# Kernel optimization log

Hardware: AMD Instinct MI355X
Metric: run time of the kernel (lower is better)

## Reference

```python
import jax, jax.numpy as jnp
import numpy as np

THETA = 10000.0

def precompute_freqs_cis(dim, seq_len):
    freqs = 1.0 / THETA ** (jnp.arange(0, dim, 2)[: dim // 2].astype(jnp.float32) / dim)
    t = jnp.arange(seq_len, dtype=jnp.float32)
    ang = jnp.outer(t, freqs)  # [T, dim/2]
    return jax.lax.complex(jnp.cos(ang), jnp.sin(ang))

def apply_rope(x, freqs_cis):
    # x: [..., T, D]; freqs_cis: [T, D/2] complex
    xr = x.astype(jnp.float32).reshape(*x.shape[:-1], -1, 2)
    xc = jax.lax.complex(xr[..., 0], xr[..., 1]) * freqs_cis
    out = jnp.stack([jnp.real(xc), jnp.imag(xc)], axis=-1).reshape(x.shape)
    return out.astype(x.dtype)

def setup_inputs() -> dict:
    key = jax.random.key(0)
    k1, k2, k3, k4 = jax.random.split(key, 4)
    B, T, E, DQ, DV = 4, 2048, 1024, 128, 128
    s = 1.0 / np.sqrt(E)
    return {
        "embedding_word": jax.random.normal(k1, (B, T, E), dtype=jnp.float32),
        "w_Q": jax.random.normal(k2, (DQ, E), dtype=jnp.float32) * s,  # torch Linear weight [out,in]
        "w_K": jax.random.normal(k3, (DQ, E), dtype=jnp.float32) * s,
        "w_V": jax.random.normal(k4, (DV, E), dtype=jnp.float32) * s,
    }

def reference(embedding_word, w_Q, w_K, w_V):
    T = embedding_word.shape[-2]
    dq = w_Q.shape[0]
    q = jnp.einsum("bte,de->btd", embedding_word, w_Q)
    k = jnp.einsum("bte,de->btd", embedding_word, w_K)
    v = jnp.einsum("bte,de->btd", embedding_word, w_V)
    fc = precompute_freqs_cis(dq, T)
    q = apply_rope(q, fc)
    k = apply_rope(k, fc)
    scores = jnp.einsum("bqd,bkd->bqk", q, k)
    causal = jnp.triu(jnp.ones((T, T), dtype=bool), k=1)
    masked = jnp.where(causal, -jnp.inf, scores)
    weights = jax.nn.softmax(masked / jnp.sqrt(jnp.float32(dq)), axis=-1)
    return jnp.einsum("bqk,bkd->bqd", weights, v)
```

## Files before the change

### kernel.cpp

```cpp
#include <hip/hip_runtime.h>
#include <math.h>


#define B_ 4
#define T_ 2048
#define E_ 1024
#define D_ 128
#define BT_ (B_ * T_)

#define UNITS_PER_B 160
#define UNITS (UNITS_PER_B * B_)

typedef __bf16 bf16_t;
typedef __bf16 bf16x4 __attribute__((ext_vector_type(4)));
typedef __bf16 bf16x8 __attribute__((ext_vector_type(8)));
typedef float f32x4 __attribute__((ext_vector_type(4)));

#define GLD16(g, l)                                                         \
  __builtin_amdgcn_global_load_lds(                                         \
      (const __attribute__((address_space(1))) void*)(g),                   \
      (__attribute__((address_space(3))) void*)(l), 16, 0, 0)

__device__ __forceinline__ bf16x8 cvt8(float4 lo, float4 hi) {
  bf16x8 t;
  t[0] = (bf16_t)lo.x; t[1] = (bf16_t)lo.y; t[2] = (bf16_t)lo.z; t[3] = (bf16_t)lo.w;
  t[4] = (bf16_t)hi.x; t[5] = (bf16_t)hi.y; t[6] = (bf16_t)hi.z; t[7] = (bf16_t)hi.w;
  return t;
}

__global__ __launch_bounds__(256) void precast_kernel(
    const float* __restrict__ X, const float* __restrict__ Wq,
    const float* __restrict__ Wk, const float* __restrict__ Wv,
    bf16_t* __restrict__ Xb, bf16_t* __restrict__ Wb,
    float2* __restrict__ Tab) {
  const int XC = BT_ * E_ / 8;
  const int WC = 3 * D_ * E_ / 8;
  for (int c = blockIdx.x * 256 + threadIdx.x; c < XC + WC;
       c += gridDim.x * 256) {
    const float* src;
    bf16_t* dst;
    if (c < XC) {
      src = X + (size_t)c * 8;
      dst = Xb + (size_t)c * 8;
    } else {
      const int cw = c - XC;
      const int z = cw / (D_ * E_ / 8);
      const int r = cw % (D_ * E_ / 8);
      src = ((z == 0) ? Wq : (z == 1) ? Wk : Wv) + (size_t)r * 8;
      dst = Wb + (size_t)z * D_ * E_ + (size_t)r * 8;
    }
    float4 u = *(const float4*)src;
    float4 v = *(const float4*)(src + 4);
    *(bf16x8*)dst = cvt8(u, v);
  }
  const float NLOG_ = -0.14391156514261485f;
  for (int idx = blockIdx.x * 256 + threadIdx.x; idx < T_ * 64;
       idx += gridDim.x * 256) {
    const int t = idx >> 6, j = idx & 63;
    const float freq = expf(NLOG_ * (float)j);
    float sn, cs;
    sincosf((float)t * freq, &sn, &cs);
    Tab[idx] = make_float2(cs, sn);
  }
}

__global__ __launch_bounds__(256) void proj64_kernel(
    const bf16_t* __restrict__ Xb, const bf16_t* __restrict__ Wb,
    const float2* __restrict__ Tab, bf16_t* __restrict__ Qws,
    bf16_t* __restrict__ Kws, bf16_t* __restrict__ Vtws) {
  const int o = blockIdx.x;
  const int ell = (o & 7) * 96 + (o >> 3);
  const int mt = ell / 6, ny = ell % 6;
  const int bt0 = mt * 64;

  const int tid = threadIdx.x;
  const int lane = tid & 63;
  const int wv = tid >> 6;
  const int wr = wv >> 1, wc = wv & 1;
  const int g = lane >> 4, lm = lane & 15;

  __shared__ bf16_t Ab[2][64 * 64];
  __shared__ bf16_t Bb[2][64 * 64];

  const bf16_t* Wz = Wb + (size_t)ny * 64 * E_;

  f32x4 acc[2][2];
#pragma unroll
  for (int m = 0; m < 2; m++)
#pragma unroll
    for (int n = 0; n < 2; n++) acc[m][n] = 0.0f;

  auto stage = [&](int t, int bf) {
    const int k0 = t * 64;
#pragma unroll
    for (int j = 0; j < 2; j++) {
      const int cb = (wv * 2 + j) * 64;
      const int c = cb + lane;
      const int row = c >> 3;
      const int eoff = ((c & 7) * 8) ^ ((row & 7) << 3);
      GLD16(Xb + (size_t)(bt0 + row) * E_ + k0 + eoff, &Ab[bf][cb * 8]);
    }
#pragma unroll
    for (int j = 0; j < 2; j++) {
      const int cb = (wv * 2 + j) * 64;
      const int c = cb + lane;
      const int row = c >> 3;
      const int eoff = ((c & 7) * 8) ^ ((row & 7) << 3);
      GLD16(Wz + (size_t)row * E_ + k0 + eoff, &Bb[bf][cb * 8]);
    }
  };

  auto compute = [&](int bf) {
#pragma unroll
    for (int ks = 0; ks < 2; ks++) {
      bf16x8 a0, a1, b0, b1;
      {
        const int r0 = wr * 32 + lm;
        a0 = *(const bf16x8*)&Ab[bf][r0 * 64 + ((ks * 32 + g * 8) ^ ((r0 & 7) << 3))];
        const int r1 = wr * 32 + 16 + lm;
        a1 = *(const bf16x8*)&Ab[bf][r1 * 64 + ((ks * 32 + g * 8) ^ ((r1 & 7) << 3))];
        const int s0 = wc * 32 + lm;
        b0 = *(const bf16x8*)&Bb[bf][s0 * 64 + ((ks * 32 + g * 8) ^ ((s0 & 7) << 3))];
        const int s1 = wc * 32 + 16 + lm;
        b1 = *(const bf16x8*)&Bb[bf][s1 * 64 + ((ks * 32 + g * 8) ^ ((s1 & 7) << 3))];
      }
      acc[0][0] = __builtin_amdgcn_mfma_f32_16x16x32_bf16(a0, b0, acc[0][0], 0, 0, 0);
      acc[0][1] = __builtin_amdgcn_mfma_f32_16x16x32_bf16(a0, b1, acc[0][1], 0, 0, 0);
      acc[1][0] = __builtin_amdgcn_mfma_f32_16x16x32_bf16(a1, b0, acc[1][0], 0, 0, 0);
      acc[1][1] = __builtin_amdgcn_mfma_f32_16x16x32_bf16(a1, b1, acc[1][1], 0, 0, 0);
    }
  };

  stage(0, 0);
  stage(1, 1);
  asm volatile("s_waitcnt vmcnt(4)" ::: "memory");
  __builtin_amdgcn_s_barrier();
  __builtin_amdgcn_sched_barrier(0);

#pragma unroll
  for (int t = 0; t < 16; t++) {
    compute(t & 1);
    __builtin_amdgcn_sched_barrier(0);
    __builtin_amdgcn_s_barrier();
    __builtin_amdgcn_sched_barrier(0);
    if (t + 2 < 16) {
      stage(t + 2, t & 1);
      asm volatile("s_waitcnt vmcnt(4)" ::: "memory");
    } else {
      asm volatile("s_waitcnt vmcnt(0)" ::: "memory");
    }
    __builtin_amdgcn_sched_barrier(0);
    __builtin_amdgcn_s_barrier();
    __builtin_amdgcn_sched_barrier(0);
  }

  const int b = bt0 >> 11;
#pragma unroll
  for (int nf = 0; nf < 2; nf++) {
    const int col = ny * 64 + wc * 32 + nf * 16 + lm;
    const int z = col >> 7;
    const int d = col & 127;
#pragma unroll
    for (int mf = 0; mf < 2; mf++) {
      const int row0 = bt0 + wr * 32 + mf * 16 + g * 4;
      if (z < 2) {
        bf16_t* dst = (z == 0) ? Qws : Kws;
#pragma unroll
        for (int r = 0; r < 4; r++) {
          const int bt = row0 + r;
          const int tt = bt & (T_ - 1);
          float val = acc[mf][nf][r];
          float prt = __shfl_xor(val, 1, 64);
          const float2 cs = Tab[(size_t)tt * 64 + (d >> 1)];
          const float outv =
              (d & 1) ? (prt * cs.y + val * cs.x) : (val * cs.x - prt * cs.y);
          dst[(size_t)bt * D_ + d] = (bf16_t)outv;
        }
      } else {
        bf16x4 pv;
#pragma unroll
        for (int r = 0; r < 4; r++) pv[r] = (bf16_t)acc[mf][nf][r];
        const int tt0 = row0 & (T_ - 1);
        *(bf16x4*)&Vtws[((size_t)(b * D_ + d)) * T_ + tt0] = pv;
      }
    }
  }
}

__global__ __launch_bounds__(128) void attn_part_kernel(
    const bf16_t* __restrict__ Qws, const bf16_t* __restrict__ Kws,
    const bf16_t* __restrict__ Vtws, float* __restrict__ Opart,
    float* __restrict__ Mpart, float* __restrict__ Lpart) {
  const int idx = blockIdx.x;
  const int b = idx / UNITS_PER_B;
  const int rem = idx % UNITS_PER_B;
  int qi, ci;
  if (rem < 16) { qi = rem; ci = 0; }
  else if (rem < 48) { int r2 = rem - 16; qi = 16 + (r2 >> 1); ci = r2 & 1; }
  else if (rem < 96) { int r2 = rem - 48; qi = 32 + r2 / 3; ci = r2 % 3; }
  else { int r2 = rem - 96; qi = 48 + (r2 >> 2); ci = r2 & 3; }
  const int slot = idx;

  const int q0 = qi * 32;
  const int tiles = (qi >> 1) + 1;
  const int t0 = ci * 8;
  const int t1 = min(t0 + 8, tiles);

  const int tid = threadIdx.x;
  const int lane = tid & 63;
  const int wv = tid >> 6;
  const int g = lane >> 4;
  const int lm = lane & 15;

  __shared__ bf16_t Ks[64 * 136];
  __shared__ bf16_t Vts[128 * 72];
  __shared__ bf16_t Ps[2 * 16 * 72];

  bf16x8 qf[4];
  {
    const bf16_t* qb = Qws + (size_t)(b * T_ + q0 + wv * 16 + lm) * D_;
#pragma unroll
    for (int kc = 0; kc < 4; kc++) qf[kc] = *(const bf16x8*)(qb + kc * 32 + g * 8);
  }

  f32x4 o[8];
#pragma unroll
  for (int i = 0; i < 8; i++) o[i] = 0.0f;
  float m_r[4], l_r[4];
#pragma unroll
  for (int r = 0; r < 4; r++) { m_r[r] = -1e30f; l_r[r] = 0.0f; }
  const float sc = 0.08838834764831845f;

  bf16x8 kreg[8], vreg[8];
  auto load_tiles = [&](int it) {
    const int k0 = it * 64;
#pragma unroll
    for (int i = 0; i < 8; i++) {
      const int c = tid + i * 128;
      kreg[i] = *(const bf16x8*)(Kws + (size_t)(b * T_ + k0 + (c >> 4)) * D_ +
                                 (c & 15) * 8);
    }
#pragma unroll
    for (int i = 0; i < 8; i++) {
      const int c = tid + i * 128;
      vreg[i] = *(const bf16x8*)(Vtws + (size_t)(b * D_ + (c >> 3)) * T_ + k0 +
                                 (c & 7) * 8);
    }
  };
  auto write_lds = [&]() {
#pragma unroll
    for (int i = 0; i < 8; i++) {
      const int c = tid + i * 128;
      *(bf16x8*)&Ks[(c >> 4) * 136 + (c & 15) * 8] = kreg[i];
    }
#pragma unroll
    for (int i = 0; i < 8; i++) {
      const int c = tid + i * 128;
      *(bf16x8*)&Vts[(c >> 3) * 72 + (c & 7) * 8] = vreg[i];
    }
  };

  load_tiles(t0);
  for (int it = t0; it < t1; it++) {
    write_lds();
    __syncthreads();
    if (it + 1 < t1) load_tiles(it + 1);

    const int k0 = it * 64;
    f32x4 s[4];
#pragma unroll
    for (int nb = 0; nb < 4; nb++) s[nb] = 0.0f;
#pragma unroll
    for (int nb = 0; nb < 4; nb++) {
#pragma unroll
      for (int kc = 0; kc < 4; kc++) {
        bf16x8 bk = *(const bf16x8*)&Ks[(nb * 16 + lm) * 136 + kc * 32 + g * 8];
        s[nb] = __builtin_amdgcn_mfma_f32_16x16x32_bf16(qf[kc], bk, s[nb], 0, 0, 0);
      }
    }

    const bool diag = (it == tiles - 1);
#pragma unroll
    for (int r = 0; r < 4; r++) {
      const int qrow = q0 + wv * 16 + g * 4 + r;
      float sv[4];
#pragma unroll
      for (int nb = 0; nb < 4; nb++) {
        sv[nb] = s[nb][r] * sc;
        if (diag && (k0 + nb * 16 + lm > qrow)) sv[nb] = -1e30f;
      }
      float tm = fmaxf(fmaxf(sv[0], sv[1]), fmaxf(sv[2], sv[3]));
      tm = fmaxf(tm, __shfl_xor(tm, 1, 64));
      tm = fmaxf(tm, __shfl_xor(tm, 2, 64));
      tm = fmaxf(tm, __shfl_xor(tm, 4, 64));
      tm = fmaxf(tm, __shfl_xor(tm, 8, 64));
      const float mnew = fmaxf(m_r[r], tm);
      const float alpha = __expf(m_r[r] - mnew);
      float p[4], rs = 0.0f;
#pragma unroll
      for (int nb = 0; nb < 4; nb++) { p[nb] = __expf(sv[nb] - mnew); rs += p[nb]; }
      rs += __shfl_xor(rs, 1, 64);
      rs += __shfl_xor(rs, 2, 64);
      rs += __shfl_xor(rs, 4, 64);
      rs += __shfl_xor(rs, 8, 64);
      l_r[r] = l_r[r] * alpha + rs;
      m_r[r] = mnew;
#pragma unroll
      for (int nb2 = 0; nb2 < 8; nb2++) o[nb2][r] *= alpha;
#pragma unroll
      for (int nb = 0; nb < 4; nb++)
        Ps[wv * 1152 + (g * 4 + r) * 72 + nb * 16 + lm] = (bf16_t)p[nb];
    }

    bf16x8 pa0 = *(const bf16x8*)&Ps[wv * 1152 + lm * 72 + g * 8];
    bf16x8 pa1 = *(const bf16x8*)&Ps[wv * 1152 + lm * 72 + 32 + g * 8];
#pragma unroll
    for (int nb2 = 0; nb2 < 8; nb2++) {
      bf16x8 bv0 = *(const bf16x8*)&Vts[(nb2 * 16 + lm) * 72 + g * 8];
      o[nb2] = __builtin_amdgcn_mfma_f32_16x16x32_bf16(pa0, bv0, o[nb2], 0, 0, 0);
      bf16x8 bv1 = *(const bf16x8*)&Vts[(nb2 * 16 + lm) * 72 + 32 + g * 8];
      o[nb2] = __builtin_amdgcn_mfma_f32_16x16x32_bf16(pa1, bv1, o[nb2], 0, 0, 0);
    }
    __syncthreads();
  }

#pragma unroll
  for (int r = 0; r < 4; r++) {
    const int row = wv * 16 + g * 4 + r;
    if (lm == 0) {
      Mpart[slot * 32 + row] = m_r[r];
      Lpart[slot * 32 + row] = l_r[r];
    }
    float* dst = Opart + ((size_t)slot * 32 + row) * D_;
#pragma unroll
    for (int nb2 = 0; nb2 < 8; nb2++) dst[nb2 * 16 + lm] = o[nb2][r];
  }
}

__global__ __launch_bounds__(256) void attn_combine_kernel(
    const float* __restrict__ Opart, const float* __restrict__ Mpart,
    const float* __restrict__ Lpart, float* __restrict__ Out) {
  const int qi = blockIdx.x;
  const int b = blockIdx.y;
  const int gg = qi >> 4;
  const int nc = gg + 1;
  const int base = b * UNITS_PER_B + ((gg * (gg + 1)) / 2) * 16 + (qi & 15) * nc;
  const int t = threadIdx.x;
  const int row = t >> 3;
  const int d0 = (t & 7) * 16;

  float mv[4];
  float mmax = -1e30f;
  for (int ci = 0; ci < nc; ci++) {
    mv[ci] = Mpart[(base + ci) * 32 + row];
    mmax = fmaxf(mmax, mv[ci]);
  }
  f32x4 acc[4];
#pragma unroll
  for (int j = 0; j < 4; j++) acc[j] = 0.0f;
  float l = 0.0f;
  for (int ci = 0; ci < nc; ci++) {
    const float w = __expf(mv[ci] - mmax);
    l += w * Lpart[(base + ci) * 32 + row];
    const float* op = Opart + ((size_t)(base + ci) * 32 + row) * D_ + d0;
#pragma unroll
    for (int j = 0; j < 4; j++) {
      float4 v = *(const float4*)(op + j * 4);
      acc[j][0] += w * v.x; acc[j][1] += w * v.y;
      acc[j][2] += w * v.z; acc[j][3] += w * v.w;
    }
  }
  const float inv = 1.0f / l;
  float* dst = Out + ((size_t)(b * T_ + qi * 32 + row)) * D_ + d0;
#pragma unroll
  for (int j = 0; j < 4; j++) {
    float4 v;
    v.x = acc[j][0] * inv; v.y = acc[j][1] * inv;
    v.z = acc[j][2] * inv; v.w = acc[j][3] * inv;
    *(float4*)(dst + j * 4) = v;
  }
}

__global__ __launch_bounds__(256) void proj_rope_kernel(
    const float* __restrict__ X, const float* __restrict__ Wq,
    const float* __restrict__ Wk, const float* __restrict__ Wv,
    bf16_t* __restrict__ Qws, bf16_t* __restrict__ Kws,
    bf16_t* __restrict__ Vtws) {
  const int z = blockIdx.y;
  const float* __restrict__ W = (z == 0) ? Wq : (z == 1) ? Wk : Wv;
  const int bt0 = blockIdx.x * 64;
  const int tid = threadIdx.x;
  const int lane = tid & 63;
  const int wv = tid >> 6;
  const int g = lane >> 4;
  const int lm = lane & 15;

  __shared__ bf16_t Xs[64 * 40];
  __shared__ bf16_t Ws[128 * 40];

  f32x4 acc[8];
#pragma unroll
  for (int i = 0; i < 8; i++) acc[i] = 0.0f;

  for (int kk = 0; kk < E_ / 32; kk++) {
    {
      const int row = tid >> 2, c0 = (tid & 3) * 8;
      const float* src = X + (size_t)(bt0 + row) * E_ + kk * 32 + c0;
      float4 u = *(const float4*)src;
      float4 v = *(const float4*)(src + 4);
      *(bf16x8*)&Xs[row * 40 + c0] = cvt8(u, v);
    }
#pragma unroll
    for (int h = 0; h < 2; h++) {
      const int cc = tid * 2 + h;
      const int row = cc >> 2, c0 = (cc & 3) * 8;
      const float* src = W + (size_t)row * E_ + kk * 32 + c0;
      float4 u = *(const float4*)src;
      float4 v = *(const float4*)(src + 4);
      *(bf16x8*)&Ws[row * 40 + c0] = cvt8(u, v);
    }
    __syncthreads();
    bf16x8 a = *(const bf16x8*)&Xs[(wv * 16 + lm) * 40 + g * 8];
#pragma unroll
    for (int nb = 0; nb < 8; nb++) {
      bf16x8 bb = *(const bf16x8*)&Ws[(nb * 16 + lm) * 40 + g * 8];
      acc[nb] = __builtin_amdgcn_mfma_f32_16x16x32_bf16(a, bb, acc[nb], 0, 0, 0);
    }
    __syncthreads();
  }
  const float NLOG_ = -0.14391156514261485f;
#pragma unroll
  for (int nb = 0; nb < 8; nb++) {
    const int col = nb * 16 + lm;
    const float freq = expf(NLOG_ * (float)(col >> 1));
#pragma unroll
    for (int r = 0; r < 4; r++) {
      const int bt = bt0 + wv * 16 + g * 4 + r;
      float val = acc[nb][r];
      float prt = __shfl_xor(val, 1, 64);
      if (z < 2) {
        const int t = bt & (T_ - 1);
        const float ang = (float)t * freq;
        float sn, cs;
        sincosf(ang, &sn, &cs);
        const float outv = (col & 1) ? (prt * sn + val * cs) : (val * cs - prt * sn);
        bf16_t* dst = (z == 0) ? Qws : Kws;
        dst[(size_t)bt * D_ + col] = (bf16_t)outv;
      } else {
        const int b = bt >> 11, t = bt & (T_ - 1);
        Vtws[((size_t)(b * D_ + col)) * T_ + t] = (bf16_t)val;
      }
    }
  }
}

__global__ __launch_bounds__(128) void attn_kernel(
    const bf16_t* __restrict__ Qws, const bf16_t* __restrict__ Kws,
    const bf16_t* __restrict__ Vtws, float* __restrict__ Out) {
  const int b = blockIdx.y;
  const int qi = blockIdx.x;
  const int q0 = qi * 32;
  const int tid = threadIdx.x;
  const int lane = tid & 63;
  const int wv = tid >> 6;
  const int g = lane >> 4;
  const int lm = lane & 15;

  __shared__ bf16_t Ks[32 * 136];
  __shared__ bf16_t Vts[128 * 40];
  __shared__ bf16_t Ps[2 * 16 * 40];

  bf16x8 qf[4];
  {
    const bf16_t* qb = Qws + (size_t)(b * T_ + q0 + wv * 16 + lm) * D_;
#pragma unroll
    for (int kk = 0; kk < 4; kk++) qf[kk] = *(const bf16x8*)(qb + kk * 32 + g * 8);
  }
  f32x4 o[8];
#pragma unroll
  for (int i = 0; i < 8; i++) o[i] = 0.0f;
  float m_r[4], l_r[4];
#pragma unroll
  for (int r = 0; r < 4; r++) { m_r[r] = -1e30f; l_r[r] = 0.0f; }
  const float sc = 0.08838834764831845f;

  for (int kt = 0; kt <= qi; kt++) {
    const int kv0 = kt * 32;
#pragma unroll
    for (int i = 0; i < 4; i++) {
      const int c = tid + i * 128;
      const int row = c >> 4, part = c & 15;
      bf16x8 v = *(const bf16x8*)(Kws + (size_t)(b * T_ + kv0 + row) * D_ + part * 8);
      *(bf16x8*)&Ks[row * 136 + part * 8] = v;
    }
#pragma unroll
    for (int i = 0; i < 4; i++) {
      const int c = tid + i * 128;
      const int d = c >> 2, part = c & 3;
      bf16x8 v = *(const bf16x8*)(Vtws + (size_t)(b * D_ + d) * T_ + kv0 + part * 8);
      *(bf16x8*)&Vts[d * 40 + part * 8] = v;
    }
    __syncthreads();
    f32x4 s[2];
    s[0] = 0.0f; s[1] = 0.0f;
#pragma unroll
    for (int nb = 0; nb < 2; nb++) {
#pragma unroll
      for (int kc = 0; kc < 4; kc++) {
        bf16x8 bk = *(const bf16x8*)&Ks[(nb * 16 + lm) * 136 + kc * 32 + g * 8];
        s[nb] = __builtin_amdgcn_mfma_f32_16x16x32_bf16(qf[kc], bk, s[nb], 0, 0, 0);
      }
    }
    const bool diag = (kt == qi);
#pragma unroll
    for (int r = 0; r < 4; r++) {
      float sv0 = s[0][r] * sc;
      float sv1 = s[1][r] * sc;
      if (diag) {
        const int rowr = wv * 16 + g * 4 + r;
        if (lm > rowr) sv0 = -1e30f;
        if (lm + 16 > rowr) sv1 = -1e30f;
      }
      float tm = fmaxf(sv0, sv1);
      tm = fmaxf(tm, __shfl_xor(tm, 1, 64));
      tm = fmaxf(tm, __shfl_xor(tm, 2, 64));
      tm = fmaxf(tm, __shfl_xor(tm, 4, 64));
      tm = fmaxf(tm, __shfl_xor(tm, 8, 64));
      const float mnew = fmaxf(m_r[r], tm);
      const float alpha = __expf(m_r[r] - mnew);
      const float p0 = __expf(sv0 - mnew);
      const float p1 = __expf(sv1 - mnew);
      float rs = p0 + p1;
      rs += __shfl_xor(rs, 1, 64);
      rs += __shfl_xor(rs, 2, 64);
      rs += __shfl_xor(rs, 4, 64);
      rs += __shfl_xor(rs, 8, 64);
      l_r[r] = l_r[r] * alpha + rs;
      m_r[r] = mnew;
#pragma unroll
      for (int nb2 = 0; nb2 < 8; nb2++) o[nb2][r] *= alpha;
      Ps[wv * 640 + (g * 4 + r) * 40 + lm] = (bf16_t)p0;
      Ps[wv * 640 + (g * 4 + r) * 40 + 16 + lm] = (bf16_t)p1;
    }
    bf16x8 pa = *(const bf16x8*)&Ps[wv * 640 + lm * 40 + g * 8];
#pragma unroll
    for (int nb2 = 0; nb2 < 8; nb2++) {
      bf16x8 bv = *(const bf16x8*)&Vts[(nb2 * 16 + lm) * 40 + g * 8];
      o[nb2] = __builtin_amdgcn_mfma_f32_16x16x32_bf16(pa, bv, o[nb2], 0, 0, 0);
    }
    __syncthreads();
  }
#pragma unroll
  for (int r = 0; r < 4; r++) {
    const float inv = 1.0f / l_r[r];
    float* dst = Out + (size_t)(b * T_ + q0 + wv * 16 + g * 4 + r) * D_;
#pragma unroll
    for (int nb2 = 0; nb2 < 8; nb2++) dst[nb2 * 16 + lm] = o[nb2][r] * inv;
  }
}

extern "C" void kernel_launch(void* const* d_in, const int* in_sizes, int n_in,
                              void* d_out, int out_size, void* d_ws,
                              size_t ws_size, hipStream_t stream) {
  const float* X = (const float*)d_in[0];
  const float* Wq = (const float*)d_in[1];
  const float* Wk = (const float*)d_in[2];
  const float* Wv = (const float*)d_in[3];
  float* Out = (float*)d_out;

  const size_t xb_bytes = (size_t)BT_ * E_ * sizeof(bf16_t);
  const size_t wb_bytes = (size_t)3 * D_ * E_ * sizeof(bf16_t);
  const size_t qkv_bytes = (size_t)3 * BT_ * D_ * sizeof(bf16_t);
  const size_t opart_bytes = (size_t)UNITS * 32 * D_ * sizeof(float);
  const size_t ml_bytes = (size_t)UNITS * 32 * sizeof(float);
  const size_t tab_bytes = (size_t)T_ * 64 * sizeof(float2);

  const size_t needA =
      xb_bytes + wb_bytes + qkv_bytes + opart_bytes + 2 * ml_bytes + tab_bytes;
  const size_t needB = qkv_bytes + opart_bytes + 2 * ml_bytes;

  if (ws_size >= needA) {
    bf16_t* Xb = (bf16_t*)d_ws;
    bf16_t* Wb = Xb + (size_t)BT_ * E_;
    bf16_t* Qws = Wb + (size_t)3 * D_ * E_;
    bf16_t* Kws = Qws + (size_t)BT_ * D_;
    bf16_t* Vtws = Kws + (size_t)BT_ * D_;
    float* Opart = (float*)((char*)d_ws + xb_bytes + wb_bytes + qkv_bytes);
    float* Mpart = (float*)((char*)Opart + opart_bytes);
    float* Lpart = (float*)((char*)Mpart + ml_bytes);
    float2* Tab = (float2*)((char*)Lpart + ml_bytes);

    hipLaunchKernelGGL(precast_kernel, dim3(2048), dim3(256), 0, stream,
                       X, Wq, Wk, Wv, Xb, Wb, Tab);
    hipLaunchKernelGGL(proj64_kernel, dim3(768), dim3(256), 0, stream,
                       Xb, Wb, Tab, Qws, Kws, Vtws);
    hipLaunchKernelGGL(attn_part_kernel, dim3(UNITS), dim3(128), 0, stream,
                       Qws, Kws, Vtws, Opart, Mpart, Lpart);
    hipLaunchKernelGGL(attn_combine_kernel, dim3(T_ / 32, B_), dim3(256), 0,
                       stream, Opart, Mpart, Lpart, Out);
  } else if (ws_size >= needB) {
    bf16_t* Qws = (bf16_t*)d_ws;
    bf16_t* Kws = Qws + (size_t)BT_ * D_;
    bf16_t* Vtws = Kws + (size_t)BT_ * D_;
    float* Opart = (float*)((char*)d_ws + qkv_bytes);
    float* Mpart = (float*)((char*)Opart + opart_bytes);
    float* Lpart = (float*)((char*)Mpart + ml_bytes);
    hipLaunchKernelGGL(proj_rope_kernel, dim3(BT_ / 64, 3), dim3(256), 0,
                       stream, X, Wq, Wk, Wv, Qws, Kws, Vtws);
    hipLaunchKernelGGL(attn_part_kernel, dim3(UNITS), dim3(128), 0, stream,
                       Qws, Kws, Vtws, Opart, Mpart, Lpart);
    hipLaunchKernelGGL(attn_combine_kernel, dim3(T_ / 32, B_), dim3(256), 0,
                       stream, Opart, Mpart, Lpart, Out);
  } else {
    bf16_t* Qws = (bf16_t*)d_ws;
    bf16_t* Kws = Qws + (size_t)BT_ * D_;
    bf16_t* Vtws = Kws + (size_t)BT_ * D_;
    hipLaunchKernelGGL(proj_rope_kernel, dim3(BT_ / 64, 3), dim3(256), 0,
                       stream, X, Wq, Wk, Wv, Qws, Kws, Vtws);
    hipLaunchKernelGGL(attn_kernel, dim3(T_ / 32, B_), dim3(128), 0, stream,
                       Qws, Kws, Vtws, Out);
  }
}
```

Measured before the change: 58.71 us.

## Fuse X fp32-to-bf16 conversion into projection GEMM staging

Removes the separate pass that converted the 32 MB fp32 activation tensor to bf16. The projection kernel now loads fp32 X tiles straight into LDS with a 16-chunk XOR swizzle and converts to bf16 when building MFMA fragments. The precast kernel is cut down to weights and the RoPE table only. In exchange, each projection block reads X in fp32 six times (once per output column tile), uses twice the LDS for the A tile, and adds conversion work to the inner loop.

```diff
diff --git a/kernel.cpp b/kernel.cpp
--- a/kernel.cpp
+++ b/kernel.cpp
@@ -27,35 +27,28 @@
   t[4] = (bf16_t)hi.x; t[5] = (bf16_t)hi.y; t[6] = (bf16_t)hi.z; t[7] = (bf16_t)hi.w;
   return t;
 }
-
-__global__ __launch_bounds__(256) void precast_kernel(
-    const float* __restrict__ X, const float* __restrict__ Wq,
-    const float* __restrict__ Wk, const float* __restrict__ Wv,
-    bf16_t* __restrict__ Xb, bf16_t* __restrict__ Wb,
+__device__ __forceinline__ bf16x8 cvt8v(f32x4 lo, f32x4 hi) {
+  bf16x8 t;
+  t[0] = (bf16_t)lo[0]; t[1] = (bf16_t)lo[1]; t[2] = (bf16_t)lo[2]; t[3] = (bf16_t)lo[3];
+  t[4] = (bf16_t)hi[0]; t[5] = (bf16_t)hi[1]; t[6] = (bf16_t)hi[2]; t[7] = (bf16_t)hi[3];
+  return t;
+}
+
+__global__ __launch_bounds__(256) void wtab_kernel(
+    const float* __restrict__ Wq, const float* __restrict__ Wk,
+    const float* __restrict__ Wv, bf16_t* __restrict__ Wb,
     float2* __restrict__ Tab) {
-  const int XC = BT_ * E_ / 8;
-  const int WC = 3 * D_ * E_ / 8;
-  for (int c = blockIdx.x * 256 + threadIdx.x; c < XC + WC;
-       c += gridDim.x * 256) {
-    const float* src;
-    bf16_t* dst;
-    if (c < XC) {
-      src = X + (size_t)c * 8;
-      dst = Xb + (size_t)c * 8;
-    } else {
-      const int cw = c - XC;
-      const int z = cw / (D_ * E_ / 8);
-      const int r = cw % (D_ * E_ / 8);
-      src = ((z == 0) ? Wq : (z == 1) ? Wk : Wv) + (size_t)r * 8;
-      dst = Wb + (size_t)z * D_ * E_ + (size_t)r * 8;
-    }
+  const int gidx = blockIdx.x * 256 + threadIdx.x;
+  if (gidx < 3 * D_ * E_ / 8) {
+    const int z = gidx / 16384;
+    const int r = gidx % 16384;
+    const float* src = ((z == 0) ? Wq : (z == 1) ? Wk : Wv) + (size_t)r * 8;
     float4 u = *(const float4*)src;
     float4 v = *(const float4*)(src + 4);
-    *(bf16x8*)dst = cvt8(u, v);
+    *(bf16x8*)(Wb + (size_t)z * D_ * E_ + (size_t)r * 8) = cvt8(u, v);
   }
   const float NLOG_ = -0.14391156514261485f;
-  for (int idx = blockIdx.x * 256 + threadIdx.x; idx < T_ * 64;
-       idx += gridDim.x * 256) {
+  for (int idx = gidx; idx < T_ * 64; idx += 65536) {
     const int t = idx >> 6, j = idx & 63;
     const float freq = expf(NLOG_ * (float)j);
     float sn, cs;
@@ -65,7 +58,7 @@
 }
 
 __global__ __launch_bounds__(256) void proj64_kernel(
-    const bf16_t* __restrict__ Xb, const bf16_t* __restrict__ Wb,
+    const float* __restrict__ X, const bf16_t* __restrict__ Wb,
     const float2* __restrict__ Tab, bf16_t* __restrict__ Qws,
     bf16_t* __restrict__ Kws, bf16_t* __restrict__ Vtws) {
   const int o = blockIdx.x;
@@ -79,7 +72,7 @@
   const int wr = wv >> 1, wc = wv & 1;
   const int g = lane >> 4, lm = lane & 15;
 
-  __shared__ bf16_t Ab[2][64 * 64];
+  __shared__ float Axf[2][64 * 64];
   __shared__ bf16_t Bb[2][64 * 64];
 
   const bf16_t* Wz = Wb + (size_t)ny * 64 * E_;
@@ -93,12 +86,13 @@
   auto stage = [&](int t, int bf) {
     const int k0 = t * 64;
 #pragma unroll
-    for (int j = 0; j < 2; j++) {
-      const int cb = (wv * 2 + j) * 64;
-      const int c = cb + lane;
-      const int row = c >> 3;
-      const int eoff = ((c & 7) * 8) ^ ((row & 7) << 3);
-      GLD16(Xb + (size_t)(bt0 + row) * E_ + k0 + eoff, &Ab[bf][cb * 8]);
+    for (int j = 0; j < 4; j++) {
+      const int cb = (wv * 4 + j) * 64;
+      const int L = cb + lane;
+      const int row = L >> 4;
+      const int pch = L & 15;
+      const int c = pch ^ (row & 15);
+      GLD16(X + (size_t)(bt0 + row) * E_ + k0 + c * 4, &Axf[bf][cb * 4]);
     }
 #pragma unroll
     for (int j = 0; j < 2; j++) {
@@ -113,12 +107,17 @@
   auto compute = [&](int bf) {
 #pragma unroll
     for (int ks = 0; ks < 2; ks++) {
+      const int cc = ks * 8 + g * 2;
       bf16x8 a0, a1, b0, b1;
       {
         const int r0 = wr * 32 + lm;
-        a0 = *(const bf16x8*)&Ab[bf][r0 * 64 + ((ks * 32 + g * 8) ^ ((r0 & 7) << 3))];
+        f32x4 lo0 = *(const f32x4*)&Axf[bf][r0 * 64 + (cc ^ (r0 & 15)) * 4];
+        f32x4 hi0 = *(const f32x4*)&Axf[bf][r0 * 64 + ((cc + 1) ^ (r0 & 15)) * 4];
+        a0 = cvt8v(lo0, hi0);
         const int r1 = wr * 32 + 16 + lm;
-        a1 = *(const bf16x8*)&Ab[bf][r1 * 64 + ((ks * 32 + g * 8) ^ ((r1 & 7) << 3))];
+        f32x4 lo1 = *(const f32x4*)&Axf[bf][r1 * 64 + (cc ^ (r1 & 15)) * 4];
+        f32x4 hi1 = *(const f32x4*)&Axf[bf][r1 * 64 + ((cc + 1) ^ (r1 & 15)) * 4];
+        a1 = cvt8v(lo1, hi1);
         const int s0 = wc * 32 + lm;
         b0 = *(const bf16x8*)&Bb[bf][s0 * 64 + ((ks * 32 + g * 8) ^ ((s0 & 7) << 3))];
         const int s1 = wc * 32 + 16 + lm;
@@ -133,7 +132,7 @@
 
   stage(0, 0);
   stage(1, 1);
-  asm volatile("s_waitcnt vmcnt(4)" ::: "memory");
+  asm volatile("s_waitcnt vmcnt(6)" ::: "memory");
   __builtin_amdgcn_s_barrier();
   __builtin_amdgcn_sched_barrier(0);
 
@@ -145,7 +144,7 @@
     __builtin_amdgcn_sched_barrier(0);
     if (t + 2 < 16) {
       stage(t + 2, t & 1);
-      asm volatile("s_waitcnt vmcnt(4)" ::: "memory");
+      asm volatile("s_waitcnt vmcnt(6)" ::: "memory");
     } else {
       asm volatile("s_waitcnt vmcnt(0)" ::: "memory");
     }
@@ -568,7 +567,6 @@
   const float* Wv = (const float*)d_in[3];
   float* Out = (float*)d_out;
 
-  const size_t xb_bytes = (size_t)BT_ * E_ * sizeof(bf16_t);
   const size_t wb_bytes = (size_t)3 * D_ * E_ * sizeof(bf16_t);
   const size_t qkv_bytes = (size_t)3 * BT_ * D_ * sizeof(bf16_t);
   const size_t opart_bytes = (size_t)UNITS * 32 * D_ * sizeof(float);
@@ -576,24 +574,23 @@
   const size_t tab_bytes = (size_t)T_ * 64 * sizeof(float2);
 
   const size_t needA =
-      xb_bytes + wb_bytes + qkv_bytes + opart_bytes + 2 * ml_bytes + tab_bytes;
+      wb_bytes + qkv_bytes + opart_bytes + 2 * ml_bytes + tab_bytes;
   const size_t needB = qkv_bytes + opart_bytes + 2 * ml_bytes;
 
   if (ws_size >= needA) {
-    bf16_t* Xb = (bf16_t*)d_ws;
-    bf16_t* Wb = Xb + (size_t)BT_ * E_;
+    bf16_t* Wb = (bf16_t*)d_ws;
     bf16_t* Qws = Wb + (size_t)3 * D_ * E_;
     bf16_t* Kws = Qws + (size_t)BT_ * D_;
     bf16_t* Vtws = Kws + (size_t)BT_ * D_;
-    float* Opart = (float*)((char*)d_ws + xb_bytes + wb_bytes + qkv_bytes);
+    float* Opart = (float*)((char*)d_ws + wb_bytes + qkv_bytes);
     float* Mpart = (float*)((char*)Opart + opart_bytes);
     float* Lpart = (float*)((char*)Mpart + ml_bytes);
     float2* Tab = (float2*)((char*)Lpart + ml_bytes);
 
-    hipLaunchKernelGGL(precast_kernel, dim3(2048), dim3(256), 0, stream,
-                       X, Wq, Wk, Wv, Xb, Wb, Tab);
+    hipLaunchKernelGGL(wtab_kernel, dim3(256), dim3(256), 0, stream,
+                       Wq, Wk, Wv, Wb, Tab);
     hipLaunchKernelGGL(proj64_kernel, dim3(768), dim3(256), 0, stream,
-                       Xb, Wb, Tab, Qws, Kws, Vtws);
+                       X, Wb, Tab, Qws, Kws, Vtws);
     hipLaunchKernelGGL(attn_part_kernel, dim3(UNITS), dim3(128), 0, stream,
                        Qws, Kws, Vtws, Opart, Mpart, Lpart);
     hipLaunchKernelGGL(attn_combine_kernel, dim3(T_ / 32, B_), dim3(256), 0,
```

New measurement: 58.38 us. About the same (-0.6%).
